# Optimization experiments

Hardware: AMD Instinct MI355X
Metric: run time of the kernel (lower is better)

## Reference

```python
import jax, jax.numpy as jnp
import numpy as np

B, T, IN = 64, 512, 3      # batch, stroke timesteps, stroke features
H = 512                    # hidden_dim
K = 10                     # num_gaussian_window
NC = 80                    # num_chars
U = 64                     # char_seq_len


def setup_inputs() -> dict:
    key = jax.random.key(0)
    ks = jax.random.split(key, 8)
    w = lambda k, sh: (jax.random.normal(k, sh, jnp.float32) * 0.05)
    return {
        "strokes": jax.random.normal(ks[0], (B, T, IN), jnp.float32),
        "sentences": jax.random.randint(ks[1], (B, U), 0, NC),
        "sentences_mask": jnp.ones((B, U), jnp.float32),
        # nn.LSTMCell params (gate order i, f, g, o)
        "W_ih": w(ks[2], (4 * H, IN + NC)),
        "W_hh": w(ks[3], (4 * H, H)),
        "b_ih": w(ks[4], (4 * H,)),
        "b_hh": w(ks[5], (4 * H,)),
        # window_layer: Linear(H, 3K)
        "W_win": w(ks[6], (3 * K, H)),
        "b_win": w(ks[7], (3 * K,)),
    }


def reference(strokes, sentences, sentences_mask, W_ih, W_hh, b_ih, b_hh, W_win, b_win):
    Bsz, Tlen, _ = strokes.shape
    Ulen = sentences.shape[-1]
    Hh = W_hh.shape[1]
    Kg = W_win.shape[0] // 3
    NCc = W_ih.shape[1] - strokes.shape[-1]
    dt = strokes.dtype

    # one_hot(sentences) * mask, precomputed once: [B, U, NC]
    C = jax.nn.one_hot(sentences, NCc, dtype=dt) * sentences_mask[..., None]
    u = jnp.arange(Ulen, dtype=dt)  # [U]

    def step(carry, x_t):
        h, c, kappa, w = carry
        inp = jnp.concatenate([x_t, w], axis=-1)              # [B, IN+NC]
        gates = inp @ W_ih.T + b_ih + h @ W_hh.T + b_hh       # [B, 4H]
        i, f, g, o = jnp.split(gates, 4, axis=-1)
        c = jax.nn.sigmoid(f) * c + jax.nn.sigmoid(i) * jnp.tanh(g)
        h = jax.nn.sigmoid(o) * jnp.tanh(c)
        p = h @ W_win.T + b_win                               # [B, 3K]
        a_hat, b_hat, k_hat = jnp.split(p, 3, axis=-1)
        alpha = jnp.exp(a_hat)
        beta = jnp.exp(b_hat)
        kappa = kappa + jnp.exp(k_hat)
        # phi[b,u] = sum_k alpha * exp(-beta * (kappa - u)^2)
        phi = jnp.einsum(
            "bk,bku->bu", alpha,
            jnp.exp(-beta[..., None] * (kappa[..., None] - u) ** 2))
        w = jnp.einsum("bu,bun->bn", phi, C)                  # [B, NC]
        return (h, c, kappa, w), (h, w)

    init = (
        jnp.zeros((Bsz, Hh), dt),
        jnp.zeros((Bsz, Hh), dt),
        jnp.zeros((Bsz, Kg), dt),
        jnp.zeros((Bsz, NCc), dt),
    )
    _, (hs, ws) = jax.lax.scan(step, init, jnp.swapaxes(strokes, 0, 1))
    # time-major -> batch-major: [B, T, H], [B, T, NC]
    return jnp.swapaxes(hs, 0, 1), jnp.swapaxes(ws, 0, 1)
```

## Files before the change

### kernel.cpp

```cpp
#include <hip/hip_runtime.h>
#include <hip/hip_bf16.h>


#define GRID_BLOCKS 64
#define TPB 256

typedef __attribute__((ext_vector_type(8))) __bf16 bf16x8;
typedef __attribute__((ext_vector_type(4))) float f32x4;
typedef __attribute__((ext_vector_type(2))) float f32x2;
typedef __attribute__((ext_vector_type(4))) int i32x4;

struct Smem {
    alignas(16) __bf16 wBf[64 * 104];
    float P[64 * 33];
    float Gt[64 * 33];
    float Al[640];
    float Be[640];
    float Ka[640];
    float Wacc[64 * 80];
    float Xt[2 * 192];
    float Maskv[4096];
    float Wx[96];
    float Bsum[32];
    float Bwin[32];
    int   Act[64];
    unsigned char Sent[4096];
};

__device__ __forceinline__ float sigf(float x) {
    return 1.f / (1.f + __expf(-x));
}
__device__ __forceinline__ float tanh_fast(float x) {
    float xx = fminf(fmaxf(x, -15.f), 15.f);
    float e = __expf(2.f * xx);
    return (e - 1.f) / (e + 1.f);
}

__global__ void init_ws_kernel(int* ws) {
    int idx = blockIdx.x * TPB + threadIdx.x;
    if (idx < 33792) ws[idx] = 0;
}

__global__ void __launch_bounds__(TPB, 1) lstm_attn(
    const float* __restrict__ strokes,
    const int*   __restrict__ sentences,
    const float* __restrict__ smask,
    const float* __restrict__ Wih,
    const float* __restrict__ Whh,
    const float* __restrict__ bih,
    const float* __restrict__ bhh,
    const float* __restrict__ Wwin,
    const float* __restrict__ bwin,
    float* __restrict__ out,
    unsigned short* __restrict__ hbuf,
    int* __restrict__ flags)
{
    __shared__ Smem S;
    const int tid  = threadIdx.x;
    const int blk  = blockIdx.x;
    const int lane = tid & 63;
    const int wave = tid >> 6;
    const int lm   = lane & 15;
    const int quad = lane >> 4;
    const int myb  = wave * 16 + lm;
    const int koff = quad * 8;

    bf16x8 rbG[2][19];
    bf16x8 rbP[2][16];
    #pragma unroll
    for (int tau = 0; tau < 2; ++tau) {
        const int colg = (lm >> 2) * 512 + blk * 8 + tau * 4 + (lm & 3);
        const float* wr = Whh + colg * 512;
        #pragma unroll
        for (int kc = 0; kc < 16; ++kc) {
            f32x4 lo = *(const f32x4*)(wr + kc * 32 + koff);
            f32x4 hi = *(const f32x4*)(wr + kc * 32 + koff + 4);
            bf16x8 b;
            b[0] = (__bf16)lo[0]; b[1] = (__bf16)lo[1];
            b[2] = (__bf16)lo[2]; b[3] = (__bf16)lo[3];
            b[4] = (__bf16)hi[0]; b[5] = (__bf16)hi[1];
            b[6] = (__bf16)hi[2]; b[7] = (__bf16)hi[3];
            rbG[tau][kc] = b;
        }
        #pragma unroll
        for (int kc = 0; kc < 3; ++kc) {
            bf16x8 b;
            #pragma unroll
            for (int j = 0; j < 8; ++j) {
                int k = kc * 32 + koff + j;
                b[j] = (__bf16)((k < 80) ? Wih[colg * 83 + 3 + k] : 0.f);
            }
            rbG[tau][16 + kc] = b;
        }
    }
    #pragma unroll
    for (int nt = 0; nt < 2; ++nt) {
        const int r = nt * 16 + lm;
        #pragma unroll
        for (int kc = 0; kc < 16; ++kc) {
            bf16x8 b;
            if (r < 30) {
                f32x4 lo = *(const f32x4*)(Wwin + r * 512 + kc * 32 + koff);
                f32x4 hi = *(const f32x4*)(Wwin + r * 512 + kc * 32 + koff + 4);
                b[0] = (__bf16)lo[0]; b[1] = (__bf16)lo[1];
                b[2] = (__bf16)lo[2]; b[3] = (__bf16)lo[3];
                b[4] = (__bf16)hi[0]; b[5] = (__bf16)hi[1];
                b[6] = (__bf16)hi[2]; b[7] = (__bf16)hi[3];
            } else {
                #pragma unroll
                for (int j = 0; j < 8; ++j) b[j] = (__bf16)0.f;
            }
            rbP[nt][kc] = b;
        }
    }

    for (int idx = tid; idx < 4096; idx += TPB) {
        S.Sent[idx]  = (unsigned char)sentences[idx];
        S.Maskv[idx] = smask[idx];
    }
    if (tid < 32) {
        int tau = tid >> 4, m = tid & 15;
        int colg = (m >> 2) * 512 + blk * 8 + tau * 4 + (m & 3);
        S.Bsum[tid] = bih[colg] + bhh[colg];
        S.Wx[tid * 3 + 0] = Wih[colg * 83 + 0];
        S.Wx[tid * 3 + 1] = Wih[colg * 83 + 1];
        S.Wx[tid * 3 + 2] = Wih[colg * 83 + 2];
        S.Bwin[tid] = (tid < 30) ? bwin[tid] : 0.f;
    }
    for (int idx = tid; idx < 640; idx += TPB) S.Ka[idx] = 0.f;
    for (int idx = tid; idx < 5120; idx += TPB) S.Wacc[idx] = 0.f;
    for (int idx = tid; idx < 64 * 104; idx += TPB) S.wBf[idx] = (__bf16)0.f;
    if (tid < 192) S.Xt[tid] = strokes[(tid / 3) * 1536 + (tid % 3)];
    float cst0 = 0.f, cst1 = 0.f;
    __syncthreads();

    const float bs0 = S.Bsum[lm], bs1 = S.Bsum[16 + lm];
    const float bw0 = S.Bwin[lm], bw1 = S.Bwin[16 + lm];
    float wx[6];
    #pragma unroll
    for (int m = 0; m < 3; ++m) {
        wx[m]     = S.Wx[lm * 3 + m];
        wx[3 + m] = S.Wx[(16 + lm) * 3 + m];
    }
    const int pb  = wave * 16 + (lane >> 2);
    const int pa2 = lane & 3;
    bool waccDirty = false;

    for (int t = 0; t <= 512; ++t) {
        if (t >= 1) {
            if (wave == 0) {
                const volatile i32x4* vf =
                    (const volatile i32x4*)((const char*)flags + lane * 64);
                for (;;) {
                    i32x4 v = *vf;
                    int m01 = v.x < v.y ? v.x : v.y;
                    int m23 = v.z < v.w ? v.z : v.w;
                    int mm  = m01 < m23 ? m01 : m23;
                    if (__all(mm >= t)) break;
                    __builtin_amdgcn_s_sleep(1);
                }
            }
            __syncthreads();
        }
        const unsigned short* hb = hbuf + ((t + 1) & 1) * 32768 + myb * 512 + koff;
        f32x4 h0,h1,h2,h3,h4,h5,h6,h7,h8,h9,h10,h11,h12,h13,h14,h15;
        asm volatile(
            "global_load_dwordx4 %0, %16, off sc0 sc1\n\t"
            "global_load_dwordx4 %1, %16, off offset:64 sc0 sc1\n\t"
            "global_load_dwordx4 %2, %16, off offset:128 sc0 sc1\n\t"
            "global_load_dwordx4 %3, %16, off offset:192 sc0 sc1\n\t"
            "global_load_dwordx4 %4, %16, off offset:256 sc0 sc1\n\t"
            "global_load_dwordx4 %5, %16, off offset:320 sc0 sc1\n\t"
            "global_load_dwordx4 %6, %16, off offset:384 sc0 sc1\n\t"
            "global_load_dwordx4 %7, %16, off offset:448 sc0 sc1\n\t"
            "global_load_dwordx4 %8, %16, off offset:512 sc0 sc1\n\t"
            "global_load_dwordx4 %9, %16, off offset:576 sc0 sc1\n\t"
            "global_load_dwordx4 %10, %16, off offset:640 sc0 sc1\n\t"
            "global_load_dwordx4 %11, %16, off offset:704 sc0 sc1\n\t"
            "global_load_dwordx4 %12, %16, off offset:768 sc0 sc1\n\t"
            "global_load_dwordx4 %13, %16, off offset:832 sc0 sc1\n\t"
            "global_load_dwordx4 %14, %16, off offset:896 sc0 sc1\n\t"
            "global_load_dwordx4 %15, %16, off offset:960 sc0 sc1\n\t"
            "s_waitcnt vmcnt(0)"
            : "=&v"(h0), "=&v"(h1), "=&v"(h2), "=&v"(h3),
              "=&v"(h4), "=&v"(h5), "=&v"(h6), "=&v"(h7),
              "=&v"(h8), "=&v"(h9), "=&v"(h10), "=&v"(h11),
              "=&v"(h12), "=&v"(h13), "=&v"(h14), "=&v"(h15)
            : "v"(hb)
            : "memory");

        f32x4 accG0 = {bs0, bs0, bs0, bs0};
        f32x4 accG1 = {bs1, bs1, bs1, bs1};
        f32x4 accP0 = {0.f, 0.f, 0.f, 0.f};
        f32x4 accP1 = {0.f, 0.f, 0.f, 0.f};
        #define KSTEP(R, I) { bf16x8 a = __builtin_bit_cast(bf16x8, R); \
            accP0 = __builtin_amdgcn_mfma_f32_16x16x32_bf16(a, rbP[0][I], accP0, 0, 0, 0); \
            accP1 = __builtin_amdgcn_mfma_f32_16x16x32_bf16(a, rbP[1][I], accP1, 0, 0, 0); \
            accG0 = __builtin_amdgcn_mfma_f32_16x16x32_bf16(a, rbG[0][I], accG0, 0, 0, 0); \
            accG1 = __builtin_amdgcn_mfma_f32_16x16x32_bf16(a, rbG[1][I], accG1, 0, 0, 0); }
        KSTEP(h0, 0)  KSTEP(h1, 1)  KSTEP(h2, 2)  KSTEP(h3, 3)
        KSTEP(h4, 4)  KSTEP(h5, 5)  KSTEP(h6, 6)  KSTEP(h7, 7)
        KSTEP(h8, 8)  KSTEP(h9, 9)  KSTEP(h10, 10) KSTEP(h11, 11)
        KSTEP(h12, 12) KSTEP(h13, 13) KSTEP(h14, 14) KSTEP(h15, 15)
        #undef KSTEP

        #pragma unroll
        for (int r = 0; r < 4; ++r) {
            int row = wave * 16 + quad * 4 + r;
            S.P[row * 33 + lm]      = accP0[r] + bw0;
            S.P[row * 33 + 16 + lm] = accP1[r] + bw1;
        }
        __builtin_amdgcn_wave_barrier();

        bool waveAny = false;
        if (t >= 1) {
            if (lane < 16) S.Act[wave * 16 + lane] = 0;
            __builtin_amdgcn_wave_barrier();
            #pragma unroll
            for (int it = 0; it < 3; ++it) {
                int idx = lane + it * 64;
                if (idx < 160) {
                    int bl = idx / 10, k = idx - bl * 10;
                    int gb = wave * 16 + bl, ad = gb * 10 + k;
                    float ka = S.Ka[ad] + __expf(S.P[gb * 33 + 20 + k]);
                    S.Ka[ad] = ka;
                    S.Al[ad] = __expf(S.P[gb * 33 + k]);
                    float be = __expf(S.P[gb * 33 + 10 + k]);
                    S.Be[ad] = be;
                    float dmin = fmaxf(fmaxf(-ka, ka - 63.f), 0.f);
                    if (be * dmin * dmin <= 36.f) atomicOr(&S.Act[gb], 1);
                }
            }
            __builtin_amdgcn_wave_barrier();
            int actv = (lane < 16) ? S.Act[wave * 16 + lane] : 0;
            waveAny = __any(actv != 0);
            if (waccDirty) {
                for (int i = lane; i < 1280; i += 64) S.Wacc[wave * 1280 + i] = 0.f;
            }
            __builtin_amdgcn_wave_barrier();
            if (waveAny) {
                #pragma unroll 1
                for (int ii = 0; ii < 16; ++ii) {
                    int gb = wave * 16 + ii;
                    if (!S.Act[gb]) continue;
                    float uu = (float)lane;
                    float s = 0.f;
                    #pragma unroll
                    for (int k = 0; k < 10; ++k) {
                        float d = S.Ka[gb * 10 + k] - uu;
                        s = fmaf(S.Al[gb * 10 + k], __expf(-S.Be[gb * 10 + k] * d * d), s);
                    }
                    float val = s * S.Maskv[gb * 64 + lane];
                    if (val != 0.f)
                        atomicAdd(&S.Wacc[gb * 80 + (int)S.Sent[gb * 64 + lane]], val);
                }
            }
            __builtin_amdgcn_wave_barrier();
            if (waveAny || waccDirty) {
                for (int i = lane; i < 1280; i += 64) {
                    int bl = i / 80, n = i - bl * 80;
                    S.wBf[(wave * 16 + bl) * 104 + n] = (__bf16)S.Wacc[wave * 1280 + i];
                }
            }
            __builtin_amdgcn_wave_barrier();
        }

        float hv0 = 0.f, hv1 = 0.f;
        if (t < 512) {
            if (waveAny) {
                const __bf16* wrow = S.wBf + myb * 104 + koff;
                #pragma unroll
                for (int kc = 0; kc < 3; ++kc) {
                    bf16x8 a = *(const bf16x8*)(wrow + kc * 32);
                    accG0 = __builtin_amdgcn_mfma_f32_16x16x32_bf16(a, rbG[0][16 + kc], accG0, 0, 0, 0);
                    accG1 = __builtin_amdgcn_mfma_f32_16x16x32_bf16(a, rbG[1][16 + kc], accG1, 0, 0, 0);
                }
            }
            const float* xb = &S.Xt[(t & 1) * 192];
            #pragma unroll
            for (int r = 0; r < 4; ++r) {
                int row = wave * 16 + quad * 4 + r;
                float x0 = xb[row * 3 + 0], x1 = xb[row * 3 + 1], x2 = xb[row * 3 + 2];
                S.Gt[row * 33 + lm]      = accG0[r] + x0 * wx[0] + x1 * wx[1] + x2 * wx[2];
                S.Gt[row * 33 + 16 + lm] = accG1[r] + x0 * wx[3] + x1 * wx[4] + x2 * wx[5];
            }
            __builtin_amdgcn_wave_barrier();
            {
                const float* g = &S.Gt[pb * 33];
                {
                    int c = 2 * pa2, tau = c >> 2, mm = c & 3;
                    const float* gg = g + tau * 16;
                    float cc = sigf(gg[4 + mm]) * cst0 + sigf(gg[mm]) * tanh_fast(gg[8 + mm]);
                    cst0 = cc;
                    hv0 = sigf(gg[12 + mm]) * tanh_fast(cc);
                }
                {
                    int c = 2 * pa2 + 1, tau = c >> 2, mm = c & 3;
                    const float* gg = g + tau * 16;
                    float cc = sigf(gg[4 + mm]) * cst1 + sigf(gg[mm]) * tanh_fast(gg[8 + mm]);
                    cst1 = cc;
                    hv1 = sigf(gg[12 + mm]) * tanh_fast(cc);
                }
                union { __bf16 q[2]; unsigned u; } pk;
                pk.q[0] = (__bf16)hv0; pk.q[1] = (__bf16)hv1;
                ((volatile unsigned*)hbuf)[(t & 1) * 16384 + pb * 256 + blk * 4 + pa2] = pk.u;
            }
            asm volatile("s_waitcnt vmcnt(0)" ::: "memory");
            if (lane == 0)
                *(volatile int*)((char*)flags + blk * 64 + wave * 4) = t + 1;
            {
                f32x2 ho = {hv0, hv1};
                *(f32x2*)(out + pb * 262144 + t * 512 + blk * 8 + 2 * pa2) = ho;
            }
            if (wave != 0 && t + 1 < 512) {
                int gi = (wave - 1) * 64 + lane;
                if (gi < 192)
                    S.Xt[((t + 1) & 1) * 192 + gi] =
                        strokes[(gi / 3) * 1536 + (t + 1) * 3 + (gi % 3)];
            }
        }
        waccDirty = waveAny;

        if (t >= 1 && wave == (blk >> 4)) {
            for (int n = lane; n < 80; n += 64)
                out[16777216 + blk * 40960 + (t - 1) * 80 + n] = S.Wacc[blk * 80 + n];
        }
    }
}

extern "C" void kernel_launch(void* const* d_in, const int* in_sizes, int n_in,
                              void* d_out, int out_size, void* d_ws, size_t ws_size,
                              hipStream_t stream) {
    const float* strokes   = (const float*)d_in[0];
    const int*   sentences = (const int*)d_in[1];
    const float* smask     = (const float*)d_in[2];
    const float* Wih       = (const float*)d_in[3];
    const float* Whh       = (const float*)d_in[4];
    const float* bih       = (const float*)d_in[5];
    const float* bhh       = (const float*)d_in[6];
    const float* Wwin      = (const float*)d_in[7];
    const float* bwin      = (const float*)d_in[8];
    float* out = (float*)d_out;
    unsigned short* hbuf = (unsigned short*)d_ws;
    int* flags = (int*)((char*)d_ws + 131072);

    init_ws_kernel<<<132, TPB, 0, stream>>>((int*)d_ws);
    lstm_attn<<<GRID_BLOCKS, TPB, 0, stream>>>(strokes, sentences, smask, Wih, Whh,
                                               bih, bhh, Wwin, bwin, out, hbuf, flags);
}
```

Measured before the change: 3.816 ms.

## Replace flag-based grid sync with timestep-tagged hidden-state words

Each 32-bit packed hidden-state value is now stored alongside its timestep tag in a 64-bit word. Consumers spin on the hidden-state loads until every tag matches the current step. This removes the separate flag polling, the waitcnt before the flag write and the block-wide __syncthreads per step. The cost is twice the hidden-state traffic per step, extra tag-checking ALU work, and reliance on 64-bit stores being atomic. Stroke prefetch is also restructured so each wave loads its own slice, which removes the cross-wave dependency on Xt.

```diff
diff --git a/kernel.cpp b/kernel.cpp
--- a/kernel.cpp
+++ b/kernel.cpp
@@ -38,7 +38,7 @@
 
 __global__ void init_ws_kernel(int* ws) {
     int idx = blockIdx.x * TPB + threadIdx.x;
-    if (idx < 33792) ws[idx] = 0;
+    if (idx < 65536) ws[idx] = 0;
 }
 
 __global__ void __launch_bounds__(TPB, 1) lstm_attn(
@@ -52,8 +52,7 @@
     const float* __restrict__ Wwin,
     const float* __restrict__ bwin,
     float* __restrict__ out,
-    unsigned short* __restrict__ hbuf,
-    int* __restrict__ flags)
+    unsigned long long* __restrict__ hbuf)
 {
     __shared__ Smem S;
     const int tid  = threadIdx.x;
@@ -130,7 +129,8 @@
     for (int idx = tid; idx < 640; idx += TPB) S.Ka[idx] = 0.f;
     for (int idx = tid; idx < 5120; idx += TPB) S.Wacc[idx] = 0.f;
     for (int idx = tid; idx < 64 * 104; idx += TPB) S.wBf[idx] = (__bf16)0.f;
-    if (tid < 192) S.Xt[tid] = strokes[(tid / 3) * 1536 + (tid % 3)];
+    const float* xsrc = strokes + (wave * 16 + lane / 3) * 1536 + (lane % 3);
+    if (lane < 48) S.Xt[wave * 48 + lane] = xsrc[0];
     float cst0 = 0.f, cst1 = 0.f;
     __syncthreads();
 
@@ -147,62 +147,37 @@
     bool waccDirty = false;
 
     for (int t = 0; t <= 512; ++t) {
-        if (t >= 1) {
-            if (wave == 0) {
-                const volatile i32x4* vf =
-                    (const volatile i32x4*)((const char*)flags + lane * 64);
-                for (;;) {
-                    i32x4 v = *vf;
-                    int m01 = v.x < v.y ? v.x : v.y;
-                    int m23 = v.z < v.w ? v.z : v.w;
-                    int mm  = m01 < m23 ? m01 : m23;
-                    if (__all(mm >= t)) break;
-                    __builtin_amdgcn_s_sleep(1);
-                }
-            }
-            __syncthreads();
-        }
-        const unsigned short* hb = hbuf + ((t + 1) & 1) * 32768 + myb * 512 + koff;
-        f32x4 h0,h1,h2,h3,h4,h5,h6,h7,h8,h9,h10,h11,h12,h13,h14,h15;
-        asm volatile(
-            "global_load_dwordx4 %0, %16, off sc0 sc1\n\t"
-            "global_load_dwordx4 %1, %16, off offset:64 sc0 sc1\n\t"
-            "global_load_dwordx4 %2, %16, off offset:128 sc0 sc1\n\t"
-            "global_load_dwordx4 %3, %16, off offset:192 sc0 sc1\n\t"
-            "global_load_dwordx4 %4, %16, off offset:256 sc0 sc1\n\t"
-            "global_load_dwordx4 %5, %16, off offset:320 sc0 sc1\n\t"
-            "global_load_dwordx4 %6, %16, off offset:384 sc0 sc1\n\t"
-            "global_load_dwordx4 %7, %16, off offset:448 sc0 sc1\n\t"
-            "global_load_dwordx4 %8, %16, off offset:512 sc0 sc1\n\t"
-            "global_load_dwordx4 %9, %16, off offset:576 sc0 sc1\n\t"
-            "global_load_dwordx4 %10, %16, off offset:640 sc0 sc1\n\t"
-            "global_load_dwordx4 %11, %16, off offset:704 sc0 sc1\n\t"
-            "global_load_dwordx4 %12, %16, off offset:768 sc0 sc1\n\t"
-            "global_load_dwordx4 %13, %16, off offset:832 sc0 sc1\n\t"
-            "global_load_dwordx4 %14, %16, off offset:896 sc0 sc1\n\t"
-            "global_load_dwordx4 %15, %16, off offset:960 sc0 sc1\n\t"
-            "s_waitcnt vmcnt(0)"
-            : "=&v"(h0), "=&v"(h1), "=&v"(h2), "=&v"(h3),
-              "=&v"(h4), "=&v"(h5), "=&v"(h6), "=&v"(h7),
-              "=&v"(h8), "=&v"(h9), "=&v"(h10), "=&v"(h11),
-              "=&v"(h12), "=&v"(h13), "=&v"(h14), "=&v"(h15)
-            : "v"(hb)
-            : "memory");
-
-        f32x4 accG0 = {bs0, bs0, bs0, bs0};
-        f32x4 accG1 = {bs1, bs1, bs1, bs1};
-        f32x4 accP0 = {0.f, 0.f, 0.f, 0.f};
-        f32x4 accP1 = {0.f, 0.f, 0.f, 0.f};
-        #define KSTEP(R, I) { bf16x8 a = __builtin_bit_cast(bf16x8, R); \
-            accP0 = __builtin_amdgcn_mfma_f32_16x16x32_bf16(a, rbP[0][I], accP0, 0, 0, 0); \
-            accP1 = __builtin_amdgcn_mfma_f32_16x16x32_bf16(a, rbP[1][I], accP1, 0, 0, 0); \
-            accG0 = __builtin_amdgcn_mfma_f32_16x16x32_bf16(a, rbG[0][I], accG0, 0, 0, 0); \
-            accG1 = __builtin_amdgcn_mfma_f32_16x16x32_bf16(a, rbG[1][I], accG1, 0, 0, 0); }
-        KSTEP(h0, 0)  KSTEP(h1, 1)  KSTEP(h2, 2)  KSTEP(h3, 3)
-        KSTEP(h4, 4)  KSTEP(h5, 5)  KSTEP(h6, 6)  KSTEP(h7, 7)
-        KSTEP(h8, 8)  KSTEP(h9, 9)  KSTEP(h10, 10) KSTEP(h11, 11)
-        KSTEP(h12, 12) KSTEP(h13, 13) KSTEP(h14, 14) KSTEP(h15, 15)
-        #undef KSTEP
+        const char* hb = (const char*)hbuf + (((t + 1) & 1) << 17) + myb * 2048 + quad * 32;
+        f32x4 accG0, accG1, accP0, accP1;
+        for (;;) {
+            i32x4 L[32];
+            #pragma unroll
+            for (int kc = 0; kc < 16; ++kc) {
+                L[2 * kc]     = *(const volatile i32x4*)(hb + kc * 128);
+                L[2 * kc + 1] = *(const volatile i32x4*)(hb + kc * 128 + 16);
+            }
+            int bad = 0;
+            #pragma unroll
+            for (int kc = 0; kc < 32; ++kc)
+                bad |= (L[kc].y ^ t) | (L[kc].w ^ t);
+            if (__builtin_expect(__all(bad == 0), 1)) {
+                accG0 = (f32x4){bs0, bs0, bs0, bs0};
+                accG1 = (f32x4){bs1, bs1, bs1, bs1};
+                accP0 = (f32x4){0.f, 0.f, 0.f, 0.f};
+                accP1 = (f32x4){0.f, 0.f, 0.f, 0.f};
+                #pragma unroll
+                for (int kc = 0; kc < 16; ++kc) {
+                    i32x4 fi = { L[2 * kc].x, L[2 * kc].z,
+                                 L[2 * kc + 1].x, L[2 * kc + 1].z };
+                    bf16x8 a = __builtin_bit_cast(bf16x8, fi);
+                    accP0 = __builtin_amdgcn_mfma_f32_16x16x32_bf16(a, rbP[0][kc], accP0, 0, 0, 0);
+                    accP1 = __builtin_amdgcn_mfma_f32_16x16x32_bf16(a, rbP[1][kc], accP1, 0, 0, 0);
+                    accG0 = __builtin_amdgcn_mfma_f32_16x16x32_bf16(a, rbG[0][kc], accG0, 0, 0, 0);
+                    accG1 = __builtin_amdgcn_mfma_f32_16x16x32_bf16(a, rbG[1][kc], accG1, 0, 0, 0);
+                }
+                break;
+            }
+        }
 
         #pragma unroll
         for (int r = 0; r < 4; ++r) {
@@ -276,11 +251,13 @@
                     accG1 = __builtin_amdgcn_mfma_f32_16x16x32_bf16(a, rbG[1][16 + kc], accG1, 0, 0, 0);
                 }
             }
-            const float* xb = &S.Xt[(t & 1) * 192];
+            const float* xb = &S.Xt[(t & 1) * 192 + wave * 48];
             #pragma unroll
             for (int r = 0; r < 4; ++r) {
                 int row = wave * 16 + quad * 4 + r;
-                float x0 = xb[row * 3 + 0], x1 = xb[row * 3 + 1], x2 = xb[row * 3 + 2];
+                float x0 = xb[(quad * 4 + r) * 3 + 0];
+                float x1 = xb[(quad * 4 + r) * 3 + 1];
+                float x2 = xb[(quad * 4 + r) * 3 + 2];
                 S.Gt[row * 33 + lm]      = accG0[r] + x0 * wx[0] + x1 * wx[1] + x2 * wx[2];
                 S.Gt[row * 33 + 16 + lm] = accG1[r] + x0 * wx[3] + x1 * wx[4] + x2 * wx[5];
             }
@@ -303,21 +280,16 @@
                 }
                 union { __bf16 q[2]; unsigned u; } pk;
                 pk.q[0] = (__bf16)hv0; pk.q[1] = (__bf16)hv1;
-                ((volatile unsigned*)hbuf)[(t & 1) * 16384 + pb * 256 + blk * 4 + pa2] = pk.u;
-            }
-            asm volatile("s_waitcnt vmcnt(0)" ::: "memory");
-            if (lane == 0)
-                *(volatile int*)((char*)flags + blk * 64 + wave * 4) = t + 1;
+                unsigned long long pv =
+                    ((unsigned long long)(unsigned)(t + 1) << 32) | (unsigned long long)pk.u;
+                ((volatile unsigned long long*)hbuf)[(t & 1) * 16384 + pb * 256 + blk * 4 + pa2] = pv;
+            }
             {
                 f32x2 ho = {hv0, hv1};
                 *(f32x2*)(out + pb * 262144 + t * 512 + blk * 8 + 2 * pa2) = ho;
             }
-            if (wave != 0 && t + 1 < 512) {
-                int gi = (wave - 1) * 64 + lane;
-                if (gi < 192)
-                    S.Xt[((t + 1) & 1) * 192 + gi] =
-                        strokes[(gi / 3) * 1536 + (t + 1) * 3 + (gi % 3)];
-            }
+            if (t + 1 < 512 && lane < 48)
+                S.Xt[((t + 1) & 1) * 192 + wave * 48 + lane] = xsrc[(t + 1) * 3];
         }
         waccDirty = waveAny;
 
@@ -341,10 +313,9 @@
     const float* Wwin      = (const float*)d_in[7];
     const float* bwin      = (const float*)d_in[8];
     float* out = (float*)d_out;
-    unsigned short* hbuf = (unsigned short*)d_ws;
-    int* flags = (int*)((char*)d_ws + 131072);
-
-    init_ws_kernel<<<132, TPB, 0, stream>>>((int*)d_ws);
+    unsigned long long* hbuf = (unsigned long long*)d_ws;
+
+    init_ws_kernel<<<256, TPB, 0, stream>>>((int*)d_ws);
     lstm_attn<<<GRID_BLOCKS, TPB, 0, stream>>>(strokes, sentences, smask, Wih, Whh,
-                                               bih, bhh, Wwin, bwin, out, hbuf, flags);
-}
+                                               bih, bhh, Wwin, bwin, out, hbuf);
+}
```

Measured after the change: 8.202 ms. 2.15x slower.

## Replace block-level flag poll plus syncthreads with per-wave flag polling

Applied to the files above, without the earlier changes.

Each wave now polls only the flags for its own 16 batch rows, with flags laid out per wave and block, instead of wave 0 polling every flag and then a block-wide __syncthreads. Stroke inputs are now prefetched per wave into wave-private slices of shared memory, so the barrier is no longer needed to order those writes. The aim is to shorten the per-timestep critical path by removing a block barrier and letting waves proceed independently. The risk is more polling traffic, since all four waves spin on global memory, and possible hazards on shared data that other waves still touch.

```diff
diff --git a/kernel.cpp b/kernel.cpp
--- a/kernel.cpp
+++ b/kernel.cpp
@@ -8,7 +8,6 @@
 typedef __attribute__((ext_vector_type(8))) __bf16 bf16x8;
 typedef __attribute__((ext_vector_type(4))) float f32x4;
 typedef __attribute__((ext_vector_type(2))) float f32x2;
-typedef __attribute__((ext_vector_type(4))) int i32x4;
 
 struct Smem {
     alignas(16) __bf16 wBf[64 * 104];
@@ -130,7 +129,8 @@
     for (int idx = tid; idx < 640; idx += TPB) S.Ka[idx] = 0.f;
     for (int idx = tid; idx < 5120; idx += TPB) S.Wacc[idx] = 0.f;
     for (int idx = tid; idx < 64 * 104; idx += TPB) S.wBf[idx] = (__bf16)0.f;
-    if (tid < 192) S.Xt[tid] = strokes[(tid / 3) * 1536 + (tid % 3)];
+    const float* xsrc = strokes + (wave * 16 + lane / 3) * 1536 + (lane % 3);
+    if (lane < 48) S.Xt[wave * 48 + lane] = xsrc[0];
     float cst0 = 0.f, cst1 = 0.f;
     __syncthreads();
 
@@ -145,22 +145,16 @@
     const int pb  = wave * 16 + (lane >> 2);
     const int pa2 = lane & 3;
     bool waccDirty = false;
+    const volatile int* pollAddr = (const volatile int*)flags + wave * 64 + lane;
+    volatile int* pubAddr = (volatile int*)flags + wave * 64 + blk;
 
     for (int t = 0; t <= 512; ++t) {
         if (t >= 1) {
-            if (wave == 0) {
-                const volatile i32x4* vf =
-                    (const volatile i32x4*)((const char*)flags + lane * 64);
-                for (;;) {
-                    i32x4 v = *vf;
-                    int m01 = v.x < v.y ? v.x : v.y;
-                    int m23 = v.z < v.w ? v.z : v.w;
-                    int mm  = m01 < m23 ? m01 : m23;
-                    if (__all(mm >= t)) break;
-                    __builtin_amdgcn_s_sleep(1);
-                }
-            }
-            __syncthreads();
+            for (;;) {
+                int v = *pollAddr;
+                if (__all(v >= t)) break;
+                __builtin_amdgcn_s_sleep(1);
+            }
         }
         const unsigned short* hb = hbuf + ((t + 1) & 1) * 32768 + myb * 512 + koff;
         f32x4 h0,h1,h2,h3,h4,h5,h6,h7,h8,h9,h10,h11,h12,h13,h14,h15;
@@ -276,11 +270,13 @@
                     accG1 = __builtin_amdgcn_mfma_f32_16x16x32_bf16(a, rbG[1][16 + kc], accG1, 0, 0, 0);
                 }
             }
-            const float* xb = &S.Xt[(t & 1) * 192];
+            const float* xb = &S.Xt[(t & 1) * 192 + wave * 48];
             #pragma unroll
             for (int r = 0; r < 4; ++r) {
                 int row = wave * 16 + quad * 4 + r;
-                float x0 = xb[row * 3 + 0], x1 = xb[row * 3 + 1], x2 = xb[row * 3 + 2];
+                float x0 = xb[(quad * 4 + r) * 3 + 0];
+                float x1 = xb[(quad * 4 + r) * 3 + 1];
+                float x2 = xb[(quad * 4 + r) * 3 + 2];
                 S.Gt[row * 33 + lm]      = accG0[r] + x0 * wx[0] + x1 * wx[1] + x2 * wx[2];
                 S.Gt[row * 33 + 16 + lm] = accG1[r] + x0 * wx[3] + x1 * wx[4] + x2 * wx[5];
             }
@@ -306,18 +302,13 @@
                 ((volatile unsigned*)hbuf)[(t & 1) * 16384 + pb * 256 + blk * 4 + pa2] = pk.u;
             }
             asm volatile("s_waitcnt vmcnt(0)" ::: "memory");
-            if (lane == 0)
-                *(volatile int*)((char*)flags + blk * 64 + wave * 4) = t + 1;
+            if (lane == 0) *pubAddr = t + 1;
             {
                 f32x2 ho = {hv0, hv1};
                 *(f32x2*)(out + pb * 262144 + t * 512 + blk * 8 + 2 * pa2) = ho;
             }
-            if (wave != 0 && t + 1 < 512) {
-                int gi = (wave - 1) * 64 + lane;
-                if (gi < 192)
-                    S.Xt[((t + 1) & 1) * 192 + gi] =
-                        strokes[(gi / 3) * 1536 + (t + 1) * 3 + (gi % 3)];
-            }
+            if (t + 1 < 512 && lane < 48)
+                S.Xt[((t + 1) & 1) * 192 + wave * 48 + lane] = xsrc[(t + 1) * 3];
         }
         waccDirty = waveAny;
 
```

Result: faster. 3.402 ms (-10.8%).
